# Optimization experiments

Hardware: AMD Instinct MI355X
Metric: run time of the kernel (lower is better)

## Reference

```python
import jax, jax.numpy as jnp
import numpy as np

HEADS = 16
DIM = 1024


def setup_inputs() -> dict:
    key = jax.random.key(0)
    ks = jax.random.split(key, 9)
    B, N, D = 2, 2048, DIM
    s = 1.0 / np.sqrt(D)
    x = jax.random.normal(ks[0], (B, N, D), dtype=jnp.float32)
    Wq = jax.random.normal(ks[1], (D, D), dtype=jnp.float32) * s
    Wk = jax.random.normal(ks[2], (D, D), dtype=jnp.float32) * s
    Wv = jax.random.normal(ks[3], (D, D), dtype=jnp.float32) * s
    Wo = jax.random.normal(ks[4], (D, D), dtype=jnp.float32) * s
    bq = jax.random.normal(ks[5], (D,), dtype=jnp.float32) * 0.01
    bk = jax.random.normal(ks[6], (D,), dtype=jnp.float32) * 0.01
    bv = jax.random.normal(ks[7], (D,), dtype=jnp.float32) * 0.01
    bo = jax.random.normal(ks[8], (D,), dtype=jnp.float32) * 0.01
    return {"x": x, "Wq": Wq, "bq": bq, "Wk": Wk, "bk": bk,
            "Wv": Wv, "bv": bv, "Wo": Wo, "bo": bo}


def reference(x, Wq, bq, Wk, bk, Wv, bv, Wo, bo):
    B, N, D = x.shape
    H = HEADS
    hd = D // H
    scale = hd ** (-0.5)
    # projections; split heads -> [B, H, N, hd]
    q = (x @ Wq + bq).reshape(B, N, H, hd).transpose(0, 2, 1, 3)
    k = (x @ Wk + bk).reshape(B, N, H, hd).transpose(0, 2, 1, 3)
    v = (x @ Wv + bv).reshape(B, N, H, hd).transpose(0, 2, 1, 3)
    # full [B, H, N, N] scores (faithful to naive torch implementation)
    attn = jnp.einsum('bhqd,bhkd->bhqk', q, k) * scale
    attn = jax.nn.softmax(attn, axis=-1)
    # dropout is identity in eval mode
    out = jnp.einsum('bhqk,bhkd->bhqd', attn, v)
    out = out.transpose(0, 2, 1, 3).reshape(B, N, D)
    return out @ Wo + bo
```

## Files before the change

### kernel.cpp

```cpp
#include <hip/hip_runtime.h>

#define HEADS 16
#define HD 64
#define SEQ 2048
#define DMODEL 1024
#define BATCH 2
#define MTOT (BATCH*SEQ)
#define KVB 64
#define NKH 16

typedef unsigned short u16;
typedef __bf16 bf16;
typedef bf16 bf16x8 __attribute__((ext_vector_type(8)));
typedef float f32x4 __attribute__((ext_vector_type(4)));
typedef float f32x16 __attribute__((ext_vector_type(16)));
typedef unsigned short u16x8 __attribute__((ext_vector_type(8)));
typedef unsigned short u16x4 __attribute__((ext_vector_type(4)));

static __device__ __forceinline__ u16 f2bf(float f) {
  bf16 b = (bf16)f;
  return __builtin_bit_cast(u16, b);
}

static __device__ __forceinline__ void async16(u16* lds_base, const u16* g) {
  __builtin_amdgcn_global_load_lds(
      (const __attribute__((address_space(1))) unsigned int*)g,
      (__attribute__((address_space(3))) unsigned int*)lds_base,
      16, 0, 0);
}

__global__ __launch_bounds__(256) void k_cvt(const float* __restrict__ in,
                                             u16* __restrict__ out, int n8) {
  int i = blockIdx.x * blockDim.x + threadIdx.x;
  if (i >= n8) return;
  const float4* p = (const float4*)(in + (size_t)i * 8);
  float4 a = p[0], b = p[1];
  u16x8 r;
  r[0] = f2bf(a.x); r[1] = f2bf(a.y); r[2] = f2bf(a.z); r[3] = f2bf(a.w);
  r[4] = f2bf(b.x); r[5] = f2bf(b.y); r[6] = f2bf(b.z); r[7] = f2bf(b.w);
  *(u16x8*)(out + (size_t)i * 8) = r;
}

__global__ __launch_bounds__(256) void k_cvtT(const float* __restrict__ W0, const float* __restrict__ W1,
                                              const float* __restrict__ W2, const float* __restrict__ W3,
                                              u16* __restrict__ T0, u16* __restrict__ T1,
                                              u16* __restrict__ T2, u16* __restrict__ T3) {
  const float* W = blockIdx.z == 0 ? W0 : blockIdx.z == 1 ? W1 : blockIdx.z == 2 ? W2 : W3;
  u16*         T = blockIdx.z == 0 ? T0 : blockIdx.z == 1 ? T1 : blockIdx.z == 2 ? T2 : T3;
  __shared__ u16 tile[64 * 68];
  int t = threadIdx.x;
  int kb = blockIdx.y * 64, nb = blockIdx.x * 64;
#pragma unroll
  for (int i = 0; i < 4; ++i) {
    int c = t * 4 + i;
    int row = c >> 4;
    int c4 = c & 15;
    float4 v = *(const float4*)&W[(size_t)(kb + row) * DMODEL + nb + c4 * 4];
    tile[row * 68 + c4 * 4 + 0] = f2bf(v.x);
    tile[row * 68 + c4 * 4 + 1] = f2bf(v.y);
    tile[row * 68 + c4 * 4 + 2] = f2bf(v.z);
    tile[row * 68 + c4 * 4 + 3] = f2bf(v.w);
  }
  __syncthreads();
#pragma unroll
  for (int i = 0; i < 2; ++i) {
    int c = t * 2 + i;
    int n = c >> 3;
    int k8 = c & 7;
    u16x8 v;
#pragma unroll
    for (int e = 0; e < 8; ++e) v[e] = tile[(k8 * 8 + e) * 68 + n];
    *(u16x8*)&T[(size_t)(nb + n) * DMODEL + kb + k8 * 8] = v;
  }
}

template <int MODE>
__global__ __launch_bounds__(256) void k_gemm(
    const u16* __restrict__ A,
    const u16* __restrict__ BT0, const u16* __restrict__ BT1, const u16* __restrict__ BT2,
    const float* __restrict__ b0, const float* __restrict__ b1, const float* __restrict__ b2,
    void* __restrict__ O0, void* __restrict__ O1, void* __restrict__ O2,
    int M, int N, int K) {
  const u16* BT = blockIdx.z == 0 ? BT0 : blockIdx.z == 1 ? BT1 : BT2;
  const float* bias = blockIdx.z == 0 ? b0 : blockIdx.z == 1 ? b1 : b2;
  void* Out = blockIdx.z == 0 ? O0 : blockIdx.z == 1 ? O1 : O2;

  __shared__ u16 Ads[2][128 * 32];
  __shared__ u16 Bds[2][128 * 32];
  int tid = threadIdx.x, wid = tid >> 6, lane = tid & 63;
  int r = lane & 15, g = lane >> 4;
  int wm = wid >> 1, wn = wid & 1;
  int m0 = blockIdx.y * 128, n0 = blockIdx.x * 128;

  f32x4 acc[4][4];
  f32x4 zero4 = {0.f, 0.f, 0.f, 0.f};
#pragma unroll
  for (int mt = 0; mt < 4; ++mt)
#pragma unroll
    for (int nt = 0; nt < 4; ++nt) acc[mt][nt] = zero4;

  int srow = lane >> 2;
  int scb = lane & 3;

  auto STAGE = [&](int b, int k0) {
#pragma unroll
    for (int tt = 0; tt < 2; ++tt) {
      int inst = wid * 2 + tt;
      int row = inst * 16 + srow;
      async16(&Ads[b][inst * 512], &A[(size_t)(m0 + row) * K + k0 + scb * 8]);
      async16(&Bds[b][inst * 512], &BT[(size_t)(n0 + row) * K + k0 + scb * 8]);
    }
  };

  auto BODY = [&](int buf, int k0) {
    if (k0 + 32 < K) STAGE(buf ^ 1, k0 + 32);
    bf16x8 af[4], bfv[4];
#pragma unroll
    for (int mt = 0; mt < 4; ++mt)
      af[mt] = *(const bf16x8*)&Ads[buf][(wm * 64 + mt * 16 + r) * 32 + g * 8];
#pragma unroll
    for (int nt = 0; nt < 4; ++nt)
      bfv[nt] = *(const bf16x8*)&Bds[buf][(wn * 64 + nt * 16 + r) * 32 + g * 8];
#pragma unroll
    for (int mt = 0; mt < 4; ++mt)
#pragma unroll
      for (int nt = 0; nt < 4; ++nt)
        acc[mt][nt] = __builtin_amdgcn_mfma_f32_16x16x32_bf16(af[mt], bfv[nt], acc[mt][nt], 0, 0, 0);
    asm volatile("s_waitcnt vmcnt(0)" ::: "memory");
    __builtin_amdgcn_sched_barrier(0);
    __builtin_amdgcn_s_barrier();
    __builtin_amdgcn_sched_barrier(0);
  };

  STAGE(0, 0);
  asm volatile("s_waitcnt vmcnt(0)" ::: "memory");
  __builtin_amdgcn_sched_barrier(0);
  __builtin_amdgcn_s_barrier();
  __builtin_amdgcn_sched_barrier(0);

  for (int k0 = 0; k0 < K; k0 += 64) {
    BODY(0, k0);
    BODY(1, k0 + 32);
  }

  const float qs = 0.18033688011112042f;
#pragma unroll
  for (int nt = 0; nt < 4; ++nt) {
    int col = n0 + wn * 64 + nt * 16 + r;
    float bv = bias[col];
#pragma unroll
    for (int mt = 0; mt < 4; ++mt) {
      int rowb = m0 + wm * 64 + mt * 16 + g * 4;
      if (MODE == 0) {
        int b = rowb >> 11;
        int h = col >> 6, d = col & (HD - 1);
        if (blockIdx.z == 2) {
          int n = rowb & (SEQ - 1);
          int np = (n & ~12) | ((n & 4) << 1) | ((n & 8) >> 1);
          u16x4 pk;
#pragma unroll
          for (int j = 0; j < 4; ++j) pk[j] = f2bf(acc[mt][nt][j] + bv);
          *(u16x4*)&((u16*)Out)[((size_t)((b * HEADS + h) * HD + d)) * SEQ + np] = pk;
        } else {
          float sc = (blockIdx.z == 0) ? qs : 1.0f;
#pragma unroll
          for (int j = 0; j < 4; ++j) {
            int row = rowb + j;
            int n = row & (SEQ - 1);
            ((u16*)Out)[((size_t)(b * HEADS + h) * SEQ + n) * HD + d] = f2bf((acc[mt][nt][j] + bv) * sc);
          }
        }
      } else {
#pragma unroll
        for (int j = 0; j < 4; ++j)
          ((float*)Out)[(size_t)(rowb + j) * N + col] = acc[mt][nt][j] + bv;
      }
    }
  }
}

__global__ __launch_bounds__(512, 4) void k_attn(const u16* __restrict__ Q,
                                                 const u16* __restrict__ Kg,
                                                 const u16* __restrict__ Vt,
                                                 u16* __restrict__ Oa) {
  __shared__ u16 lds[2][2][2][KVB * 64];

  int tid = threadIdx.x, wid = tid >> 6, lane = tid & 63;
  int l31 = lane & 31, hi = lane >> 5;
  int h = wid >> 2, s = wid & 3;

  int fid = blockIdx.y * gridDim.x + blockIdx.x;
  int swz = (fid & 7) * 64 + (fid >> 3);
  int qt = swz & 15;
  int bh = swz >> 4;

  const size_t kbase = (size_t)bh * SEQ * HD;
  const size_t vbase = (size_t)bh * HD * SEQ;
  int q0 = qt * 128 + s * 32;

  bf16x8 qf[4];
#pragma unroll
  for (int db = 0; db < 4; ++db)
    qf[db] = *(const bf16x8*)&Q[kbase + (size_t)(q0 + l31) * HD + db * 16 + hi * 8];

  int swz7 = l31 & 7;
  int coff[4];
#pragma unroll
  for (int i = 0; i < 4; ++i) coff[i] = ((2 * i + hi) ^ swz7) * 8;

  f32x16 zero16 = {0.f,0.f,0.f,0.f,0.f,0.f,0.f,0.f,0.f,0.f,0.f,0.f,0.f,0.f,0.f,0.f};
  f32x16 oacc0 = zero16, oacc1 = zero16, lacc = zero16;

  u16x8 onesb;
#pragma unroll
  for (int e = 0; e < 8; ++e) onesb[e] = 0x3F80;
  bf16x8 ones = __builtin_bit_cast(bf16x8, onesb);

  auto STAGE = [&](int b, int kc) {
    int kof = (h * NKH + kc) * KVB;
#pragma unroll
    for (int i = 0; i < 2; ++i) {
      int inst = s * 2 + i;
      int rr = inst * 8 + (lane >> 3);
      int ch = (lane & 7) ^ (rr & 7);
      async16(&lds[b][h][0][inst * 512], &Kg[kbase + (size_t)(kof + rr) * HD + ch * 8]);
      async16(&lds[b][h][1][inst * 512], &Vt[vbase + (size_t)rr * SEQ + kof + ch * 8]);
    }
  };

  auto BODY = [&](int buf, int kc) {
    if (kc + 1 < NKH) STAGE(buf ^ 1, kc + 1);

    const u16* Kb = &lds[buf][h][0][0];
    const u16* Vb = &lds[buf][h][1][0];

    f32x16 s0 = zero16, s1 = zero16;
    __builtin_amdgcn_s_setprio(1);
#pragma unroll
    for (int db = 0; db < 4; ++db) {
      bf16x8 kf0 = *(const bf16x8*)&Kb[l31 * 64 + coff[db]];
      bf16x8 kf1 = *(const bf16x8*)&Kb[2048 + l31 * 64 + coff[db]];
      s0 = __builtin_amdgcn_mfma_f32_32x32x16_bf16(kf0, qf[db], s0, 0, 0, 0);
      s1 = __builtin_amdgcn_mfma_f32_32x32x16_bf16(kf1, qf[db], s1, 0, 0, 0);
    }
    __builtin_amdgcn_s_setprio(0);

#pragma unroll
    for (int t = 0; t < 4; ++t) {
      u16x8 pk8;
#pragma unroll
      for (int e = 0; e < 8; ++e) {
        float sv = (t & 2) ? ((t & 1) ? s1[8 + e] : s1[e])
                           : ((t & 1) ? s0[8 + e] : s0[e]);
        pk8[e] = f2bf(__builtin_amdgcn_exp2f(sv));
      }
      bf16x8 pa = __builtin_bit_cast(bf16x8, pk8);

      bf16x8 vf0 = *(const bf16x8*)&Vb[l31 * 64 + coff[t]];
      bf16x8 vf1 = *(const bf16x8*)&Vb[2048 + l31 * 64 + coff[t]];
      __builtin_amdgcn_s_setprio(1);
      lacc  = __builtin_amdgcn_mfma_f32_32x32x16_bf16(pa, ones, lacc, 0, 0, 0);
      oacc0 = __builtin_amdgcn_mfma_f32_32x32x16_bf16(pa, vf0, oacc0, 0, 0, 0);
      oacc1 = __builtin_amdgcn_mfma_f32_32x32x16_bf16(pa, vf1, oacc1, 0, 0, 0);
      __builtin_amdgcn_s_setprio(0);
    }

    asm volatile("s_waitcnt vmcnt(0)" ::: "memory");
    __builtin_amdgcn_sched_barrier(0);
    __builtin_amdgcn_s_barrier();
    __builtin_amdgcn_sched_barrier(0);
  };

  STAGE(0, 0);
  asm volatile("s_waitcnt vmcnt(0)" ::: "memory");
  __builtin_amdgcn_sched_barrier(0);
  __builtin_amdgcn_s_barrier();
  __builtin_amdgcn_sched_barrier(0);

  for (int kc = 0; kc < NKH; kc += 2) {
    BODY(0, kc);
    BODY(1, kc + 1);
  }

  float* cf = (float*)&lds[0][0][0][0];
  if (h == 1) {
#pragma unroll
    for (int r = 0; r < 16; ++r) {
      cf[s * 3072 + r * 64 + lane] = oacc0[r];
      cf[s * 3072 + 1024 + r * 64 + lane] = oacc1[r];
      cf[s * 3072 + 2048 + r * 64 + lane] = lacc[r];
    }
  }
  __syncthreads();
  if (h == 0) {
#pragma unroll
    for (int r = 0; r < 16; ++r) {
      oacc0[r] += cf[s * 3072 + r * 64 + lane];
      oacc1[r] += cf[s * 3072 + 1024 + r * 64 + lane];
      lacc[r]  += cf[s * 3072 + 2048 + r * 64 + lane];
    }
    int b = bh >> 4, hh = bh & 15;
#pragma unroll
    for (int reg = 0; reg < 16; ++reg) {
      int q = q0 + (reg & 3) + 8 * (reg >> 2) + 4 * hi;
      float inv = 1.0f / lacc[reg];
      size_t rowoff = ((size_t)(b * SEQ + q)) * DMODEL + hh * HD;
      Oa[rowoff + l31]      = f2bf(oacc0[reg] * inv);
      Oa[rowoff + 32 + l31] = f2bf(oacc1[reg] * inv);
    }
  }
}

extern "C" void kernel_launch(void* const* d_in, const int* in_sizes, int n_in,
                              void* d_out, int out_size, void* d_ws, size_t ws_size,
                              hipStream_t stream) {
  const float* x  = (const float*)d_in[0];
  const float* Wq = (const float*)d_in[1];
  const float* bq = (const float*)d_in[2];
  const float* Wk = (const float*)d_in[3];
  const float* bk = (const float*)d_in[4];
  const float* Wv = (const float*)d_in[5];
  const float* bv = (const float*)d_in[6];
  const float* Wo = (const float*)d_in[7];
  const float* bo = (const float*)d_in[8];

  char* ws = (char*)d_ws;
  const size_t MB = 1024 * 1024;
  u16* xb    = (u16*)(ws);
  u16* wqT   = (u16*)(ws + 8 * MB);
  u16* wkT   = (u16*)(ws + 10 * MB);
  u16* wvT   = (u16*)(ws + 12 * MB);
  u16* woT   = (u16*)(ws + 14 * MB);
  u16* qbuf  = (u16*)(ws + 16 * MB);
  u16* kbuf  = (u16*)(ws + 24 * MB);
  u16* vbufT = (u16*)(ws + 32 * MB);
  u16* abuf  = (u16*)(ws + 40 * MB);

  k_cvt<<<2048, 256, 0, stream>>>(x, xb, (MTOT * DMODEL) / 8);
  k_cvtT<<<dim3(16, 16, 4), 256, 0, stream>>>(Wq, Wk, Wv, Wo, wqT, wkT, wvT, woT);
  k_gemm<0><<<dim3(DMODEL / 128, MTOT / 128, 3), 256, 0, stream>>>(
      xb, wqT, wkT, wvT, bq, bk, bv, qbuf, kbuf, vbufT, MTOT, DMODEL, DMODEL);
  k_attn<<<dim3(SEQ / 128, BATCH * HEADS), 512, 0, stream>>>(qbuf, kbuf, vbufT, abuf);
  k_gemm<1><<<dim3(DMODEL / 128, MTOT / 128, 1), 256, 0, stream>>>(
      abuf, woT, woT, woT, bo, bo, bo, d_out, d_out, d_out, MTOT, DMODEL, DMODEL);
}
```

Before: 118.7 us.

## Process two query tiles per wave in attention to reuse K/V fragments

Each attention wave now computes 64 query rows instead of 32, sharing every K and V LDS fragment across two MFMA tiles, and the grid is halved accordingly. This cuts LDS traffic and K/V staging per query and amortizes per-block setup. In exchange, register use roughly doubles, launch bounds drop to 2 blocks per CU, and fewer blocks means less latency hiding. The setprio hints are also removed, and the epilogue reduces the two tiles sequentially through LDS.

```diff
diff --git a/kernel.cpp b/kernel.cpp
--- a/kernel.cpp
+++ b/kernel.cpp
@@ -179,7 +179,7 @@
   }
 }
 
-__global__ __launch_bounds__(512, 4) void k_attn(const u16* __restrict__ Q,
+__global__ __launch_bounds__(512, 2) void k_attn(const u16* __restrict__ Q,
                                                  const u16* __restrict__ Kg,
                                                  const u16* __restrict__ Vt,
                                                  u16* __restrict__ Oa) {
@@ -190,18 +190,20 @@
   int h = wid >> 2, s = wid & 3;
 
   int fid = blockIdx.y * gridDim.x + blockIdx.x;
-  int swz = (fid & 7) * 64 + (fid >> 3);
-  int qt = swz & 15;
-  int bh = swz >> 4;
+  int swz = (fid & 7) * 32 + (fid >> 3);
+  int qt = swz & 7;
+  int bh = swz >> 3;
 
   const size_t kbase = (size_t)bh * SEQ * HD;
   const size_t vbase = (size_t)bh * HD * SEQ;
-  int q0 = qt * 128 + s * 32;
-
-  bf16x8 qf[4];
-#pragma unroll
-  for (int db = 0; db < 4; ++db)
-    qf[db] = *(const bf16x8*)&Q[kbase + (size_t)(q0 + l31) * HD + db * 16 + hi * 8];
+  int qA = qt * 256 + s * 64;
+
+  bf16x8 qfA[4], qfB[4];
+#pragma unroll
+  for (int db = 0; db < 4; ++db) {
+    qfA[db] = *(const bf16x8*)&Q[kbase + (size_t)(qA + l31) * HD + db * 16 + hi * 8];
+    qfB[db] = *(const bf16x8*)&Q[kbase + (size_t)(qA + 32 + l31) * HD + db * 16 + hi * 8];
+  }
 
   int swz7 = l31 & 7;
   int coff[4];
@@ -209,7 +211,8 @@
   for (int i = 0; i < 4; ++i) coff[i] = ((2 * i + hi) ^ swz7) * 8;
 
   f32x16 zero16 = {0.f,0.f,0.f,0.f,0.f,0.f,0.f,0.f,0.f,0.f,0.f,0.f,0.f,0.f,0.f,0.f};
-  f32x16 oacc0 = zero16, oacc1 = zero16, lacc = zero16;
+  f32x16 oa0A = zero16, oa1A = zero16, lA = zero16;
+  f32x16 oa0B = zero16, oa1B = zero16, lB = zero16;
 
   u16x8 onesb;
 #pragma unroll
@@ -234,35 +237,40 @@
     const u16* Kb = &lds[buf][h][0][0];
     const u16* Vb = &lds[buf][h][1][0];
 
-    f32x16 s0 = zero16, s1 = zero16;
-    __builtin_amdgcn_s_setprio(1);
+    f32x16 s0A = zero16, s1A = zero16, s0B = zero16, s1B = zero16;
 #pragma unroll
     for (int db = 0; db < 4; ++db) {
       bf16x8 kf0 = *(const bf16x8*)&Kb[l31 * 64 + coff[db]];
       bf16x8 kf1 = *(const bf16x8*)&Kb[2048 + l31 * 64 + coff[db]];
-      s0 = __builtin_amdgcn_mfma_f32_32x32x16_bf16(kf0, qf[db], s0, 0, 0, 0);
-      s1 = __builtin_amdgcn_mfma_f32_32x32x16_bf16(kf1, qf[db], s1, 0, 0, 0);
-    }
-    __builtin_amdgcn_s_setprio(0);
+      s0A = __builtin_amdgcn_mfma_f32_32x32x16_bf16(kf0, qfA[db], s0A, 0, 0, 0);
+      s1A = __builtin_amdgcn_mfma_f32_32x32x16_bf16(kf1, qfA[db], s1A, 0, 0, 0);
+      s0B = __builtin_amdgcn_mfma_f32_32x32x16_bf16(kf0, qfB[db], s0B, 0, 0, 0);
+      s1B = __builtin_amdgcn_mfma_f32_32x32x16_bf16(kf1, qfB[db], s1B, 0, 0, 0);
+    }
 
 #pragma unroll
     for (int t = 0; t < 4; ++t) {
-      u16x8 pk8;
+      u16x8 pkA, pkB;
 #pragma unroll
       for (int e = 0; e < 8; ++e) {
-        float sv = (t & 2) ? ((t & 1) ? s1[8 + e] : s1[e])
-                           : ((t & 1) ? s0[8 + e] : s0[e]);
-        pk8[e] = f2bf(__builtin_amdgcn_exp2f(sv));
+        float svA = (t & 2) ? ((t & 1) ? s1A[8 + e] : s1A[e])
+                            : ((t & 1) ? s0A[8 + e] : s0A[e]);
+        float svB = (t & 2) ? ((t & 1) ? s1B[8 + e] : s1B[e])
+                            : ((t & 1) ? s0B[8 + e] : s0B[e]);
+        pkA[e] = f2bf(__builtin_amdgcn_exp2f(svA));
+        pkB[e] = f2bf(__builtin_amdgcn_exp2f(svB));
       }
-      bf16x8 pa = __builtin_bit_cast(bf16x8, pk8);
+      bf16x8 paA = __builtin_bit_cast(bf16x8, pkA);
+      bf16x8 paB = __builtin_bit_cast(bf16x8, pkB);
 
       bf16x8 vf0 = *(const bf16x8*)&Vb[l31 * 64 + coff[t]];
       bf16x8 vf1 = *(const bf16x8*)&Vb[2048 + l31 * 64 + coff[t]];
-      __builtin_amdgcn_s_setprio(1);
-      lacc  = __builtin_amdgcn_mfma_f32_32x32x16_bf16(pa, ones, lacc, 0, 0, 0);
-      oacc0 = __builtin_amdgcn_mfma_f32_32x32x16_bf16(pa, vf0, oacc0, 0, 0, 0);
-      oacc1 = __builtin_amdgcn_mfma_f32_32x32x16_bf16(pa, vf1, oacc1, 0, 0, 0);
-      __builtin_amdgcn_s_setprio(0);
+      lA   = __builtin_amdgcn_mfma_f32_32x32x16_bf16(paA, ones, lA, 0, 0, 0);
+      oa0A = __builtin_amdgcn_mfma_f32_32x32x16_bf16(paA, vf0, oa0A, 0, 0, 0);
+      oa1A = __builtin_amdgcn_mfma_f32_32x32x16_bf16(paA, vf1, oa1A, 0, 0, 0);
+      lB   = __builtin_amdgcn_mfma_f32_32x32x16_bf16(paB, ones, lB, 0, 0, 0);
+      oa0B = __builtin_amdgcn_mfma_f32_32x32x16_bf16(paB, vf0, oa0B, 0, 0, 0);
+      oa1B = __builtin_amdgcn_mfma_f32_32x32x16_bf16(paB, vf1, oa1B, 0, 0, 0);
     }
 
     asm volatile("s_waitcnt vmcnt(0)" ::: "memory");
@@ -283,30 +291,51 @@
   }
 
   float* cf = (float*)&lds[0][0][0][0];
+  int b = bh >> 4, hh = bh & 15;
+
   if (h == 1) {
 #pragma unroll
     for (int r = 0; r < 16; ++r) {
-      cf[s * 3072 + r * 64 + lane] = oacc0[r];
-      cf[s * 3072 + 1024 + r * 64 + lane] = oacc1[r];
-      cf[s * 3072 + 2048 + r * 64 + lane] = lacc[r];
+      cf[s * 3072 + r * 64 + lane]        = oa0A[r];
+      cf[s * 3072 + 1024 + r * 64 + lane] = oa1A[r];
+      cf[s * 3072 + 2048 + r * 64 + lane] = lA[r];
     }
   }
   __syncthreads();
   if (h == 0) {
 #pragma unroll
+    for (int reg = 0; reg < 16; ++reg) {
+      float o0 = oa0A[reg] + cf[s * 3072 + reg * 64 + lane];
+      float o1 = oa1A[reg] + cf[s * 3072 + 1024 + reg * 64 + lane];
+      float lv = lA[reg]   + cf[s * 3072 + 2048 + reg * 64 + lane];
+      float inv = 1.0f / lv;
+      int q = qA + (reg & 3) + 8 * (reg >> 2) + 4 * hi;
+      size_t rowoff = ((size_t)(b * SEQ + q)) * DMODEL + hh * HD;
+      Oa[rowoff + l31]      = f2bf(o0 * inv);
+      Oa[rowoff + 32 + l31] = f2bf(o1 * inv);
+    }
+  }
+  __syncthreads();
+  if (h == 1) {
+#pragma unroll
     for (int r = 0; r < 16; ++r) {
-      oacc0[r] += cf[s * 3072 + r * 64 + lane];
-      oacc1[r] += cf[s * 3072 + 1024 + r * 64 + lane];
-      lacc[r]  += cf[s * 3072 + 2048 + r * 64 + lane];
-    }
-    int b = bh >> 4, hh = bh & 15;
+      cf[s * 3072 + r * 64 + lane]        = oa0B[r];
+      cf[s * 3072 + 1024 + r * 64 + lane] = oa1B[r];
+      cf[s * 3072 + 2048 + r * 64 + lane] = lB[r];
+    }
+  }
+  __syncthreads();
+  if (h == 0) {
 #pragma unroll
     for (int reg = 0; reg < 16; ++reg) {
-      int q = q0 + (reg & 3) + 8 * (reg >> 2) + 4 * hi;
-      float inv = 1.0f / lacc[reg];
+      float o0 = oa0B[reg] + cf[s * 3072 + reg * 64 + lane];
+      float o1 = oa1B[reg] + cf[s * 3072 + 1024 + reg * 64 + lane];
+      float lv = lB[reg]   + cf[s * 3072 + 2048 + reg * 64 + lane];
+      float inv = 1.0f / lv;
+      int q = qA + 32 + (reg & 3) + 8 * (reg >> 2) + 4 * hi;
       size_t rowoff = ((size_t)(b * SEQ + q)) * DMODEL + hh * HD;
-      Oa[rowoff + l31]      = f2bf(oacc0[reg] * inv);
-      Oa[rowoff + 32 + l31] = f2bf(oacc1[reg] * inv);
+      Oa[rowoff + l31]      = f2bf(o0 * inv);
+      Oa[rowoff + 32 + l31] = f2bf(o1 * inv);
     }
   }
 }
@@ -340,7 +369,7 @@
   k_cvtT<<<dim3(16, 16, 4), 256, 0, stream>>>(Wq, Wk, Wv, Wo, wqT, wkT, wvT, woT);
   k_gemm<0><<<dim3(DMODEL / 128, MTOT / 128, 3), 256, 0, stream>>>(
       xb, wqT, wkT, wvT, bq, bk, bv, qbuf, kbuf, vbufT, MTOT, DMODEL, DMODEL);
-  k_attn<<<dim3(SEQ / 128, BATCH * HEADS), 512, 0, stream>>>(qbuf, kbuf, vbufT, abuf);
+  k_attn<<<dim3(SEQ / 256, BATCH * HEADS), 512, 0, stream>>>(qbuf, kbuf, vbufT, abuf);
   k_gemm<1><<<dim3(DMODEL / 128, MTOT / 128, 1), 256, 0, stream>>>(
       abuf, woT, woT, woT, bo, bo, bo, d_out, d_out, d_out, MTOT, DMODEL, DMODEL);
 }
```

Measured after the change: 111.2 us. 6.4% less time.
